# Optimization experiments

Hardware: AMD Instinct MI355X
Metric: run time of the kernel (lower is better)

Reference implementation:

```python
import jax, jax.numpy as jnp
import numpy as np

D_MODEL = 1024
N_STATE = 64
BASEWIDTH = 3
BC_SCALE = (D_MODEL / BASEWIDTH) ** -0.5  # 'mup' mode width_mult**-0.5
RMS_EPS = 1.1920928955078125e-07  # torch.finfo(float32).eps (RMSNorm eps=None default)


def setup_inputs() -> dict:
    key = jax.random.key(0)
    k1, k2, k3, k4 = jax.random.split(key, 4)
    Bsz, L = 4, 2048
    u = jax.random.normal(k1, (Bsz, D_MODEL, L), dtype=jnp.float32)
    A = jax.random.uniform(k2, (N_STATE,), dtype=jnp.float32) * 0.1  # buffer: rand(N)*A_scale
    B = (jax.random.normal(k3, (N_STATE, D_MODEL), dtype=jnp.float32) + 0.1) * BC_SCALE
    C = (jax.random.normal(k4, (N_STATE, D_MODEL), dtype=jnp.float32) + 0.1) * BC_SCALE
    D = jnp.ones((D_MODEL,), dtype=jnp.float32)
    norm_w = jnp.ones((D_MODEL,), dtype=jnp.float32)
    return {"L": L, "u": u, "A": A, "B": B, "C": C, "D": D, "norm_w": norm_w}


def _ssm(u, A, B, C, D, norm_w):
    # u: [b, d, l]
    scale = BC_SCALE  # applied to Bu, Cu in 'mup' hyperparam mode
    Bu = jnp.einsum('nd,bdl->bnl', B, u) * scale  # [b, n, l]
    Cu = jnp.einsum('nd,bdl->bnl', C, u) * scale  # [b, n, l]
    b, d, l = u.shape
    # shifted_delta == 1 (delta path commented out in source), so
    # h_{t} = A * h_{t-1} + Bu[:, :, t] (outer) u[:, :, t]
    h0 = jnp.zeros((b, d, A.shape[0]), dtype=u.dtype)

    def step(h, xs):
        bu_t, cu_t, u_t = xs  # [b,n], [b,n], [b,d]
        h = h * A + u_t[:, :, None] * bu_t[:, None, :]  # [b, d, n]
        y_t = jnp.einsum('bn,bdn->bd', cu_t, h)
        return h, y_t

    xs = (jnp.moveaxis(Bu, 2, 0), jnp.moveaxis(Cu, 2, 0), jnp.moveaxis(u, 2, 0))
    _, y = jax.lax.scan(step, h0, xs)  # y: [l, b, d]
    y = jnp.moveaxis(y, 0, 2).transpose(1, 0, 2) if False else jnp.transpose(y, (1, 2, 0))  # [b, d, l]
    out = y + u * D[None, :, None]
    # RMSNorm over d_model (apply in [b, l, d] layout)
    x = jnp.transpose(out, (0, 2, 1))  # [b, l, d]
    ms = jnp.mean(x * x, axis=-1, keepdims=True)
    x = x * jax.lax.rsqrt(ms + RMS_EPS) * norm_w
    return jnp.transpose(x, (0, 2, 1))  # [b, d, l]


def reference(L, u, A, B, C, D, norm_w):
    del L  # sequence length == u.shape[-1]
    return _ssm(u, A, B, C, D, norm_w)
```

## Files before the change

### kernel.cpp

```cpp
#include <hip/hip_runtime.h>
#include <stdint.h>

#define DM 1024
#define LS 2048
#define RMS_EPS 1.1920928955078125e-07f
#define S2 0.0029296875f

typedef __attribute__((ext_vector_type(8))) short bf16x8;
typedef __attribute__((ext_vector_type(4))) float f32x4;

__device__ __forceinline__ unsigned short f2bf(float f) {
  uint32_t u = __builtin_bit_cast(uint32_t, f);
  u += 0x7FFFu + ((u >> 16) & 1u);
  return (unsigned short)(u >> 16);
}

__global__ __launch_bounds__(256) void k0_prep(const float* __restrict__ B,
                                               const float* __restrict__ C,
                                               unsigned short* __restrict__ Bbf) {
  int i4 = blockIdx.x * 256 + threadIdx.x;
  const float4* src = (i4 < 16384) ? (const float4*)B : (const float4*)C;
  float4 v = src[i4 & 16383];
  ushort4 o;
  o.x = f2bf(v.x); o.y = f2bf(v.y); o.z = f2bf(v.z); o.w = f2bf(v.w);
  ((ushort4*)Bbf)[i4] = o;
}

__global__ __launch_bounds__(256) void k1_gemm(const float* __restrict__ u,
                                               const unsigned short* __restrict__ Bbf,
                                               float* __restrict__ BuCuT) {
  const int b  = blockIdx.y;
  const int l0 = blockIdx.x * 32;
  const int lane = threadIdx.x & 63;
  const int w    = threadIdx.x >> 6;
  const int n = lane & 15;
  const int q = lane >> 4;
  const float* ub = u + (size_t)b * DM * LS;

  f32x4 acc[2][2] = {};
  #pragma unroll 2
  for (int k0 = 0; k0 < DM; k0 += 32) {
    bf16x8 a[2], bb[2];
    #pragma unroll
    for (int rt = 0; rt < 2; ++rt) {
      int row = 32*w + 16*rt + n;
      a[rt] = *(const bf16x8*)(Bbf + (size_t)row * DM + k0 + 8*q);
    }
    #pragma unroll
    for (int ct = 0; ct < 2; ++ct) {
      int col = l0 + 16*ct + n;
      union { bf16x8 v; unsigned short s[8]; } t;
      #pragma unroll
      for (int j = 0; j < 8; ++j)
        t.s[j] = f2bf(ub[(size_t)(k0 + 8*q + j) * LS + col]);
      bb[ct] = t.v;
    }
    #pragma unroll
    for (int rt = 0; rt < 2; ++rt)
      #pragma unroll
      for (int ct = 0; ct < 2; ++ct)
        acc[rt][ct] = __builtin_amdgcn_mfma_f32_16x16x32_bf16(a[rt], bb[ct], acc[rt][ct], 0, 0, 0);
  }
  float* ob = BuCuT + (size_t)b * LS * 128;
  #pragma unroll
  for (int rt = 0; rt < 2; ++rt)
    #pragma unroll
    for (int ct = 0; ct < 2; ++ct) {
      int col = l0 + 16*ct + n;
      int row = 32*w + 16*rt + 4*q;
      *(f32x4*)(ob + (size_t)col * 128 + row) = acc[rt][ct];
    }
}

__global__ __launch_bounds__(256) void k2_kw(const float* __restrict__ BuCuT,
                                             const float* __restrict__ A,
                                             float* __restrict__ Kw) {
  const int b  = blockIdx.y;
  const int t0 = blockIdx.x * 64;
  const int tl = threadIdx.x >> 2;
  const int p  = threadIdx.x & 3;
  const int t  = t0 + tl;
  const float* base = BuCuT + (size_t)b * LS * 128;

  float pw[16], aa[16];
  #pragma unroll
  for (int i = 0; i < 4; ++i) {
    float4 c4 = *(const float4*)(base + (size_t)t * 128 + 64 + 16*p + 4*i);
    float4 a4 = *(const float4*)(A + 16*p + 4*i);
    pw[4*i+0] = c4.x * S2; aa[4*i+0] = a4.x;
    pw[4*i+1] = c4.y * S2; aa[4*i+1] = a4.y;
    pw[4*i+2] = c4.z * S2; aa[4*i+2] = a4.z;
    pw[4*i+3] = c4.w * S2; aa[4*i+3] = a4.w;
  }
  float part[16];
  #pragma unroll
  for (int j = 0; j < 16; ++j) {
    float s = 0.f;
    if (t - j >= 0) {
      const float* bu = base + (size_t)(t - j) * 128 + 16*p;
      #pragma unroll
      for (int i = 0; i < 16; i += 4) {
        float4 b4 = *(const float4*)(bu + i);
        s = fmaf(pw[i+0], b4.x, s); s = fmaf(pw[i+1], b4.y, s);
        s = fmaf(pw[i+2], b4.z, s); s = fmaf(pw[i+3], b4.w, s);
      }
    }
    part[j] = s;
    #pragma unroll
    for (int i = 0; i < 16; ++i) pw[i] *= aa[i];
  }
  __shared__ float ss[64][68];
  #pragma unroll
  for (int j = 0; j < 16; ++j) ss[tl][p*17 + j] = part[j];
  __syncthreads();
  const int o  = threadIdx.x * 4;
  const int t2 = o >> 4;
  const int j0 = o & 15;
  float4 r;
  r.x = ss[t2][j0+0] + ss[t2][17+j0+0] + ss[t2][34+j0+0] + ss[t2][51+j0+0];
  r.y = ss[t2][j0+1] + ss[t2][17+j0+1] + ss[t2][34+j0+1] + ss[t2][51+j0+1];
  r.z = ss[t2][j0+2] + ss[t2][17+j0+2] + ss[t2][34+j0+2] + ss[t2][51+j0+2];
  r.w = ss[t2][j0+3] + ss[t2][17+j0+3] + ss[t2][34+j0+3] + ss[t2][51+j0+3];
  *(float4*)(Kw + ((size_t)b * LS + t0 + t2) * 16 + j0) = r;
}

__global__ __launch_bounds__(256) void k3_conv(const float* __restrict__ u,
                                               const float* __restrict__ Kw,
                                               const float* __restrict__ Dv,
                                               const float* __restrict__ nw,
                                               float* __restrict__ out) {
  const int b  = blockIdx.y;
  const int t0 = blockIdx.x * 16;
  const int tg = threadIdx.x & 3;
  const int dr = threadIdx.x >> 2;
  const float* ub = u + (size_t)b * DM * LS;
  float* ob = out + (size_t)b * DM * LS;

  float kw[4][16];
  #pragma unroll
  for (int k = 0; k < 4; ++k) {
    const float* kp = Kw + ((size_t)b * LS + t0 + 4*tg + k) * 16;
    #pragma unroll
    for (int i = 0; i < 4; ++i) {
      float4 v = *(const float4*)(kp + 4*i);
      kw[k][4*i+0] = v.x; kw[k][4*i+1] = v.y; kw[k][4*i+2] = v.z; kw[k][4*i+3] = v.w;
    }
  }

  const int cbase = t0 - 16 + 4*tg;
  float y[16][4];
  float ps[4] = {0.f, 0.f, 0.f, 0.f};
  #pragma unroll
  for (int c = 0; c < 16; ++c) {
    const int d = dr + 64*c;
    const float* row = ub + (size_t)d * LS;
    float wr[20];
    #pragma unroll
    for (int s5 = 0; s5 < 5; ++s5) {
      int g = cbase + 4*s5;
      float4 v;
      if (g >= 0) v = *(const float4*)(row + g);
      else        v = make_float4(0.f, 0.f, 0.f, 0.f);
      wr[4*s5+0] = v.x; wr[4*s5+1] = v.y; wr[4*s5+2] = v.z; wr[4*s5+3] = v.w;
    }
    const float Dd = Dv[d];
    #pragma unroll
    for (int k = 0; k < 4; ++k) {
      float acc = wr[16+k] * Dd;
      #pragma unroll
      for (int j = 0; j < 16; ++j)
        acc = fmaf(kw[k][j], wr[16 + k - j], acc);
      y[c][k] = acc;
      ps[k] = fmaf(acc, acc, ps[k]);
    }
  }

  __shared__ float ss[16][68];
  #pragma unroll
  for (int k = 0; k < 4; ++k) ss[4*tg + k][dr] = ps[k];
  __syncthreads();
  __shared__ float rsq[16];
  if (threadIdx.x < 16) {
    float s = 0.f;
    #pragma unroll
    for (int i = 0; i < 16; ++i) {
      float4 v = *(const float4*)&ss[threadIdx.x][4*i];
      s += (v.x + v.y) + (v.z + v.w);
    }
    rsq[threadIdx.x] = rsqrtf(s * (1.f/1024.f) + RMS_EPS);
  }
  __syncthreads();
  float rq[4];
  #pragma unroll
  for (int k = 0; k < 4; ++k) rq[k] = rsq[4*tg + k];
  #pragma unroll
  for (int c = 0; c < 16; ++c) {
    const int d = dr + 64*c;
    const float wn = nw[d];
    float4 o;
    o.x = y[c][0] * rq[0] * wn;
    o.y = y[c][1] * rq[1] * wn;
    o.z = y[c][2] * rq[2] * wn;
    o.w = y[c][3] * rq[3] * wn;
    *(float4*)(ob + (size_t)d * LS + t0 + 4*tg) = o;
  }
}

extern "C" void kernel_launch(void* const* d_in, const int* in_sizes, int n_in,
                              void* d_out, int out_size, void* d_ws, size_t ws_size,
                              hipStream_t stream) {
  const float* u  = (const float*)d_in[1];
  const float* A  = (const float*)d_in[2];
  const float* B  = (const float*)d_in[3];
  const float* C  = (const float*)d_in[4];
  const float* Dv = (const float*)d_in[5];
  const float* nw = (const float*)d_in[6];
  float* out = (float*)d_out;

  float* BuCuT = (float*)d_ws;
  float* Kw    = (float*)((char*)d_ws + (4u << 20));
  unsigned short* Bbf = (unsigned short*)((char*)d_ws + (4u << 20) + (512u << 10));

  k0_prep<<<dim3(128),    dim3(256), 0, stream>>>(B, C, Bbf);
  k1_gemm<<<dim3(64, 4),  dim3(256), 0, stream>>>(u, Bbf, BuCuT);
  k2_kw  <<<dim3(32, 4),  dim3(256), 0, stream>>>(BuCuT, A, Kw);
  k3_conv<<<dim3(128, 4), dim3(256), 0, stream>>>(u, Kw, Dv, nw, out);
}
```

Measured before the change: 143.1 us.

## Stage u tile in LDS as bf16 with coalesced float4 loads in projection GEMM

The projection GEMM now loads each block's full 1024x16 slice of u once, using coalesced float4 reads. It converts the slice to bf16 and stores it in a swizzled shared-memory tile, and the MFMA loop then reads B fragments from LDS. Previously every thread did strided scalar global loads of u per k-step. The l-tile shrinks from 32 to 16 columns, so the grid doubles to 512 blocks for more parallelism, and each block issues half as many MFMAs per A-fragment load. In exchange, the bf16 weight matrix is now re-read from global memory twice as often.

```diff
diff --git a/kernel.cpp b/kernel.cpp
--- a/kernel.cpp
+++ b/kernel.cpp
@@ -29,47 +29,57 @@
 __global__ __launch_bounds__(256) void k1_gemm(const float* __restrict__ u,
                                                const unsigned short* __restrict__ Bbf,
                                                float* __restrict__ BuCuT) {
-  const int b  = blockIdx.y;
-  const int l0 = blockIdx.x * 32;
+  const int b    = blockIdx.y;
+  const int l0   = blockIdx.x * 16;
   const int lane = threadIdx.x & 63;
   const int w    = threadIdx.x >> 6;
+  const float* ub = u + (size_t)b * DM * LS;
+
+  __shared__ bf16x8 tile[128][16];
+
+  {
+    const int lq = lane & 3;
+    const int kg = lane >> 2;
+    const int kbase = 256 * w + 16 * kg;
+    #pragma unroll
+    for (int h = 0; h < 2; ++h) {
+      float4 vv[8];
+      #pragma unroll
+      for (int r = 0; r < 8; ++r)
+        vv[r] = *(const float4*)(ub + (size_t)(kbase + 8*h + r) * LS + l0 + 4*lq);
+      const int k8 = 32*w + 2*kg + h;
+      #pragma unroll
+      for (int c = 0; c < 4; ++c) {
+        union { bf16x8 v; unsigned short s[8]; } t;
+        #pragma unroll
+        for (int r = 0; r < 8; ++r) t.s[r] = f2bf(((const float*)&vv[r])[c]);
+        tile[k8][(4*lq + c) ^ (k8 & 3)] = t.v;
+      }
+    }
+  }
+  __syncthreads();
+
   const int n = lane & 15;
   const int q = lane >> 4;
-  const float* ub = u + (size_t)b * DM * LS;
-
-  f32x4 acc[2][2] = {};
-  #pragma unroll 2
-  for (int k0 = 0; k0 < DM; k0 += 32) {
-    bf16x8 a[2], bb[2];
+  f32x4 acc[2] = {};
+  #pragma unroll 4
+  for (int it = 0; it < 32; ++it) {
+    bf16x8 bfrag = tile[4*it + q][n ^ q];
     #pragma unroll
     for (int rt = 0; rt < 2; ++rt) {
       int row = 32*w + 16*rt + n;
-      a[rt] = *(const bf16x8*)(Bbf + (size_t)row * DM + k0 + 8*q);
-    }
-    #pragma unroll
-    for (int ct = 0; ct < 2; ++ct) {
-      int col = l0 + 16*ct + n;
-      union { bf16x8 v; unsigned short s[8]; } t;
-      #pragma unroll
-      for (int j = 0; j < 8; ++j)
-        t.s[j] = f2bf(ub[(size_t)(k0 + 8*q + j) * LS + col]);
-      bb[ct] = t.v;
-    }
-    #pragma unroll
-    for (int rt = 0; rt < 2; ++rt)
-      #pragma unroll
-      for (int ct = 0; ct < 2; ++ct)
-        acc[rt][ct] = __builtin_amdgcn_mfma_f32_16x16x32_bf16(a[rt], bb[ct], acc[rt][ct], 0, 0, 0);
-  }
+      bf16x8 a = *(const bf16x8*)(Bbf + (size_t)row * DM + 32*it + 8*q);
+      acc[rt] = __builtin_amdgcn_mfma_f32_16x16x32_bf16(a, bfrag, acc[rt], 0, 0, 0);
+    }
+  }
+
   float* ob = BuCuT + (size_t)b * LS * 128;
   #pragma unroll
-  for (int rt = 0; rt < 2; ++rt)
-    #pragma unroll
-    for (int ct = 0; ct < 2; ++ct) {
-      int col = l0 + 16*ct + n;
-      int row = 32*w + 16*rt + 4*q;
-      *(f32x4*)(ob + (size_t)col * 128 + row) = acc[rt][ct];
-    }
+  for (int rt = 0; rt < 2; ++rt) {
+    int col = l0 + n;
+    int row = 32*w + 16*rt + 4*q;
+    *(f32x4*)(ob + (size_t)col * 128 + row) = acc[rt];
+  }
 }
 
 __global__ __launch_bounds__(256) void k2_kw(const float* __restrict__ BuCuT,
@@ -222,7 +232,7 @@
   unsigned short* Bbf = (unsigned short*)((char*)d_ws + (4u << 20) + (512u << 10));
 
   k0_prep<<<dim3(128),    dim3(256), 0, stream>>>(B, C, Bbf);
-  k1_gemm<<<dim3(64, 4),  dim3(256), 0, stream>>>(u, Bbf, BuCuT);
+  k1_gemm<<<dim3(128, 4), dim3(256), 0, stream>>>(u, Bbf, BuCuT);
   k2_kw  <<<dim3(32, 4),  dim3(256), 0, stream>>>(BuCuT, A, Kw);
   k3_conv<<<dim3(128, 4), dim3(256), 0, stream>>>(u, Kw, Dv, nw, out);
 }
```

Result: slower. 155.5 us (+8.7%).
